# Kernel optimization log

Measured on AMD Instinct MI355X. Metric: run time of the kernel, lower is better.

## Reference

```python
import jax, jax.numpy as jnp
import numpy as np


def setup_inputs() -> dict:
    key = jax.random.key(0)
    k1, k2, k3, k4, k5 = jax.random.split(key, 5)
    B, N, E, C, O = 4, 10000, 32, 128, 128
    x = jax.random.normal(k1, (B, N, C), dtype=jnp.float32)
    idx = jax.random.randint(k2, (B, N, E), 0, N)
    drop = jax.random.uniform(k3, (B, N, E)) < 0.1
    edge_index = jnp.where(drop, -1, idx).astype(jnp.int64)
    W = jax.random.normal(k4, (2 * C, O), dtype=jnp.float32) * (1.0 / np.sqrt(2 * C))
    b = jax.random.normal(k5, (O,), dtype=jnp.float32) * 0.01
    return {"x": x, "edge_index": edge_index, "W": W, "b": b}


def reference(x, edge_index, W, b):
    B, N, C = x.shape
    E = edge_index.shape[-1]
    # pad a zero node row; -1 indices point at it (torch negative-index semantics)
    padded = jnp.concatenate([x, jnp.zeros((B, 1, C), dtype=x.dtype)], axis=1)  # [B, N+1, C]
    idx = jnp.where(edge_index < 0, N, edge_index)
    neigh = jax.vmap(lambda p, i: p[i])(padded, idx)  # [B, N, E, C]
    x_e = jnp.broadcast_to(x[:, :, None, :], (B, N, E, C))
    feat = jnp.concatenate([x_e, neigh - x_e], axis=-1)  # [B, N, E, 2C]
    h = jax.nn.elu(jnp.einsum('bnec,co->bneo', feat, W) + b)  # [B, N, E, O]
    h = jnp.where((edge_index != -1)[..., None], h, -jnp.inf)
    return jnp.max(h, axis=2)  # [B, N, O]
```

## Files before the change

### kernel.cpp

```cpp
#include <hip/hip_runtime.h>
#include <math.h>

#define BATCH 4
#define NNODE 10000
#define EDIM  32
#define CDIM  128
#define ODIM  128
#define MTOT  (BATCH * NNODE)

typedef __attribute__((ext_vector_type(8))) short bf16x8;
typedef __attribute__((ext_vector_type(4))) float f32x4;

__device__ __forceinline__ unsigned short f2bf(float f) {
    unsigned u = __float_as_uint(f);
    u += 0x7fffu + ((u >> 16) & 1u);
    return (unsigned short)(u >> 16);
}
__device__ __forceinline__ float bf2f(unsigned short h) {
    return __uint_as_float(((unsigned)h) << 16);
}

__global__ __launch_bounds__(256) void prep_w(
    const float* __restrict__ W, unsigned short* __restrict__ Bcat,
    unsigned short* __restrict__ Tsent)
{
    int gid = blockIdx.x * 256 + threadIdx.x;
    int n = gid >> 7;
    int k = gid & 127;
    float v;
    if (n < 128) v = W[(size_t)k * ODIM + n] - W[(size_t)(k + 128) * ODIM + n];
    else         v = W[(size_t)(k + 128) * ODIM + (n - 128)];
    Bcat[(size_t)n * CDIM + k] = f2bf(v);
    if (gid < ODIM) Tsent[gid] = 0xFF80;
}

__global__ __launch_bounds__(256) void gemm_mfma(
    const float* __restrict__ x,
    const unsigned short* __restrict__ Bcat,
    const float* __restrict__ bias,
    unsigned short* __restrict__ U,
    unsigned short* __restrict__ T)
{
    __shared__ char lds_raw[32 * 132 * 4];
    unsigned short* As = (unsigned short*)lds_raw;
    float*          Cf = (float*)lds_raw;

    const int tid  = threadIdx.x;
    const int m0   = blockIdx.x * 32;
    const int wv   = tid >> 6;
    const int lane = tid & 63;
    const int l16  = lane & 15;
    const int quad = lane >> 4;
    const int nq   = wv * 64;

    #pragma unroll
    for (int i = 0; i < 4; i++) {
        int lin = i * 256 + tid;
        int row = lin >> 5;
        int f4  = lin & 31;
        float4 v = *(const float4*)&x[(size_t)(m0 + row) * CDIM + f4 * 4];
        ushort4 h;
        h.x = f2bf(v.x); h.y = f2bf(v.y); h.z = f2bf(v.z); h.w = f2bf(v.w);
        int kblk = f4 >> 1, half = f4 & 1;
        *(ushort4*)((char*)As + row * 256 + (((kblk ^ (row & 15)) << 4) + half * 8)) = h;
    }
    __syncthreads();

    f32x4 acc[2][4];
    #pragma unroll
    for (int i = 0; i < 2; i++)
        #pragma unroll
        for (int j = 0; j < 4; j++) acc[i][j] = (f32x4){0.f, 0.f, 0.f, 0.f};

    #pragma unroll
    for (int ks = 0; ks < 4; ks++) {
        const int kb = ks * 32 + quad * 8;

        bf16x8 bfr[4];
        #pragma unroll
        for (int ct = 0; ct < 4; ct++)
            bfr[ct] = *(const bf16x8*)(Bcat + (size_t)(nq + ct * 16 + l16) * CDIM + kb);

        bf16x8 afr[2];
        #pragma unroll
        for (int rt = 0; rt < 2; rt++) {
            int row  = rt * 16 + l16;
            int kblk = ks * 4 + quad;
            afr[rt] = *(const bf16x8*)((char*)As + row * 256 + ((kblk ^ l16) << 4));
        }

        #pragma unroll
        for (int rt = 0; rt < 2; rt++)
            #pragma unroll
            for (int ct = 0; ct < 4; ct++)
                acc[rt][ct] = __builtin_amdgcn_mfma_f32_16x16x32_bf16(
                    afr[rt], bfr[ct], acc[rt][ct], 0, 0, 0);
    }

    __syncthreads();
    if (wv < 2) {
        #pragma unroll
        for (int rt = 0; rt < 2; rt++)
            #pragma unroll
            for (int ct = 0; ct < 4; ct++)
                #pragma unroll
                for (int r = 0; r < 4; r++)
                    Cf[(rt * 16 + quad * 4 + r) * 132 + nq + ct * 16 + l16] = acc[rt][ct][r];
    }
    __syncthreads();
    #pragma unroll
    for (int i = 0; i < 4; i++) {
        int lin = i * 256 + tid;
        int row = lin >> 5, f4 = lin & 31;
        float4 v  = *(const float4*)&Cf[row * 132 + f4 * 4];
        float4 bb = *(const float4*)&bias[f4 * 4];
        ushort4 h;
        h.x = f2bf(v.x + bb.x); h.y = f2bf(v.y + bb.y);
        h.z = f2bf(v.z + bb.z); h.w = f2bf(v.w + bb.w);
        *(ushort4*)&U[(size_t)(m0 + row) * ODIM + f4 * 4] = h;
    }
    __syncthreads();
    if (wv >= 2) {
        #pragma unroll
        for (int rt = 0; rt < 2; rt++)
            #pragma unroll
            for (int ct = 0; ct < 4; ct++)
                #pragma unroll
                for (int r = 0; r < 4; r++)
                    Cf[(rt * 16 + quad * 4 + r) * 132 + (nq - 128) + ct * 16 + l16] = acc[rt][ct][r];
    }
    __syncthreads();
    #pragma unroll
    for (int i = 0; i < 4; i++) {
        int lin = i * 256 + tid;
        int row = lin >> 5, f4 = lin & 31;
        float4 v = *(const float4*)&Cf[row * 132 + f4 * 4];
        ushort4 h;
        h.x = f2bf(v.x); h.y = f2bf(v.y); h.z = f2bf(v.z); h.w = f2bf(v.w);
        *(ushort4*)&T[(size_t)(m0 + row) * ODIM + f4 * 4] = h;
    }
}

__global__ __launch_bounds__(256) void gather_max(
    const int* __restrict__ idx,
    const unsigned short* __restrict__ Ub,
    const unsigned short* __restrict__ T,
    float* __restrict__ out)
{
    __shared__ int sidx[16][EDIM];

    const int g   = blockIdx.x;
    const int b   = g & 3;
    const int nb0 = (g >> 2) * 16;
    const int tid = threadIdx.x;
    const int sent = NNODE * (BATCH - b);

    #pragma unroll
    for (int i = 0; i < 2; i++) {
        int lin = i * 256 + tid;
        int n = lin >> 5, e = lin & 31;
        int j = idx[(size_t)(b * NNODE + nb0 + n) * EDIM + e];
        sidx[n][e] = (j < 0) ? sent : j;
    }
    __syncthreads();

    const int wv   = tid >> 6;
    const int lane = tid & 63;
    const int q4   = lane >> 4;
    const int l16  = lane & 15;
    const int myn  = wv * 4 + q4;
    const int node = b * NNODE + nb0 + myn;
    const unsigned short* tb = T + (size_t)b * NNODE * ODIM;
    const int o8 = l16 * 8;

    uint4 uraw = *(const uint4*)(Ub + (size_t)node * ODIM + o8);

    float m[8];
    #pragma unroll
    for (int i = 0; i < 8; i++) m[i] = -INFINITY;

    #pragma unroll
    for (int e0 = 0; e0 < EDIM; e0 += 16) {
        uint4 v[16];
        #pragma unroll
        for (int q = 0; q < 16; q++) {
            int j = sidx[myn][e0 + q];
            v[q] = *(const uint4*)(tb + (size_t)j * ODIM + o8);
        }
        #pragma unroll
        for (int q = 0; q < 16; q++) {
            m[0] = fmaxf(m[0], __uint_as_float(v[q].x << 16));
            m[1] = fmaxf(m[1], __uint_as_float(v[q].x & 0xffff0000u));
            m[2] = fmaxf(m[2], __uint_as_float(v[q].y << 16));
            m[3] = fmaxf(m[3], __uint_as_float(v[q].y & 0xffff0000u));
            m[4] = fmaxf(m[4], __uint_as_float(v[q].z << 16));
            m[5] = fmaxf(m[5], __uint_as_float(v[q].z & 0xffff0000u));
            m[6] = fmaxf(m[6], __uint_as_float(v[q].w << 16));
            m[7] = fmaxf(m[7], __uint_as_float(v[q].w & 0xffff0000u));
        }
    }

    const bool any = m[0] > -INFINITY;
    float uu[8];
    uu[0] = bf2f((unsigned short)(uraw.x & 0xffff)); uu[1] = bf2f((unsigned short)(uraw.x >> 16));
    uu[2] = bf2f((unsigned short)(uraw.y & 0xffff)); uu[3] = bf2f((unsigned short)(uraw.y >> 16));
    uu[4] = bf2f((unsigned short)(uraw.z & 0xffff)); uu[5] = bf2f((unsigned short)(uraw.z >> 16));
    uu[6] = bf2f((unsigned short)(uraw.w & 0xffff)); uu[7] = bf2f((unsigned short)(uraw.w >> 16));
    float r[8];
    #pragma unroll
    for (int i = 0; i < 8; i++) {
        float s = uu[i] + m[i];
        r[i] = any ? (s > 0.f ? s : __expf(s) - 1.f) : -INFINITY;
    }
    *(float4*)&out[(size_t)node * ODIM + o8]     = make_float4(r[0], r[1], r[2], r[3]);
    *(float4*)&out[(size_t)node * ODIM + o8 + 4] = make_float4(r[4], r[5], r[6], r[7]);
}

extern "C" void kernel_launch(void* const* d_in, const int* in_sizes, int n_in,
                              void* d_out, int out_size, void* d_ws, size_t ws_size,
                              hipStream_t stream) {
    const float* x    = (const float*)d_in[0];
    const int*   idx  = (const int*)d_in[1];
    const float* W    = (const float*)d_in[2];
    const float* bias = (const float*)d_in[3];
    float* out        = (float*)d_out;

    const size_t tBytes = (size_t)(MTOT + 1) * ODIM * sizeof(unsigned short);
    const size_t uBytes = (size_t)MTOT * ODIM * sizeof(unsigned short);
    unsigned short* T    = (unsigned short*)d_ws;
    unsigned short* U    = (unsigned short*)((char*)d_ws + tBytes);
    unsigned short* Bcat = (unsigned short*)((char*)d_ws + tBytes + uBytes);
    unsigned short* Tsent = T + (size_t)MTOT * ODIM;

    prep_w    <<<128,        256, 0, stream>>>(W, Bcat, Tsent);
    gemm_mfma <<<MTOT / 32,  256, 0, stream>>>(x, Bcat, bias, U, T);
    gather_max<<<MTOT / 16,  256, 0, stream>>>(idx, U, T, out);
}
```

Before: 111.3 us.

## Store GEMM results straight from MFMA registers and use packed f16 max in gather

```diff
diff --git a/kernel.cpp b/kernel.cpp
--- a/kernel.cpp
+++ b/kernel.cpp
@@ -11,6 +11,8 @@
 typedef __attribute__((ext_vector_type(8))) short bf16x8;
 typedef __attribute__((ext_vector_type(4))) float f32x4;
 
+#define SENT_BF16 0xFBFFu
+
 __device__ __forceinline__ unsigned short f2bf(float f) {
     unsigned u = __float_as_uint(f);
     u += 0x7fffu + ((u >> 16) & 1u);
@@ -18,6 +20,9 @@
 }
 __device__ __forceinline__ float bf2f(unsigned short h) {
     return __uint_as_float(((unsigned)h) << 16);
+}
+__device__ __forceinline__ void pkmax(unsigned& acc, unsigned v) {
+    asm("v_pk_max_f16 %0, %0, %1" : "+v"(acc) : "v"(v));
 }
 
 __global__ __launch_bounds__(256) void prep_w(
@@ -31,7 +36,7 @@
     if (n < 128) v = W[(size_t)k * ODIM + n] - W[(size_t)(k + 128) * ODIM + n];
     else         v = W[(size_t)(k + 128) * ODIM + (n - 128)];
     Bcat[(size_t)n * CDIM + k] = f2bf(v);
-    if (gid < ODIM) Tsent[gid] = 0xFF80;
+    if (gid < ODIM) Tsent[gid] = (unsigned short)SENT_BF16;
 }
 
 __global__ __launch_bounds__(256) void gemm_mfma(
@@ -41,9 +46,7 @@
     unsigned short* __restrict__ U,
     unsigned short* __restrict__ T)
 {
-    __shared__ char lds_raw[32 * 132 * 4];
-    unsigned short* As = (unsigned short*)lds_raw;
-    float*          Cf = (float*)lds_raw;
+    __shared__ unsigned short As[32 * 128];
 
     const int tid  = threadIdx.x;
     const int m0   = blockIdx.x * 32;
@@ -76,17 +79,17 @@
     for (int ks = 0; ks < 4; ks++) {
         const int kb = ks * 32 + quad * 8;
 
-        bf16x8 bfr[4];
+        bf16x8 wfr[4];
         #pragma unroll
         for (int ct = 0; ct < 4; ct++)
-            bfr[ct] = *(const bf16x8*)(Bcat + (size_t)(nq + ct * 16 + l16) * CDIM + kb);
-
-        bf16x8 afr[2];
+            wfr[ct] = *(const bf16x8*)(Bcat + (size_t)(nq + ct * 16 + l16) * CDIM + kb);
+
+        bf16x8 xfr[2];
         #pragma unroll
         for (int rt = 0; rt < 2; rt++) {
             int row  = rt * 16 + l16;
             int kblk = ks * 4 + quad;
-            afr[rt] = *(const bf16x8*)((char*)As + row * 256 + ((kblk ^ l16) << 4));
+            xfr[rt] = *(const bf16x8*)((char*)As + row * 256 + ((kblk ^ l16) << 4));
         }
 
         #pragma unroll
@@ -94,50 +97,40 @@
             #pragma unroll
             for (int ct = 0; ct < 4; ct++)
                 acc[rt][ct] = __builtin_amdgcn_mfma_f32_16x16x32_bf16(
-                    afr[rt], bfr[ct], acc[rt][ct], 0, 0, 0);
-    }
-
-    __syncthreads();
+                    wfr[ct], xfr[rt], acc[rt][ct], 0, 0, 0);
+    }
+
     if (wv < 2) {
         #pragma unroll
-        for (int rt = 0; rt < 2; rt++)
+        for (int ct = 0; ct < 4; ct++) {
+            int c0 = nq + ct * 16 + quad * 4;
+            float4 b4 = *(const float4*)&bias[c0];
             #pragma unroll
-            for (int ct = 0; ct < 4; ct++)
-                #pragma unroll
-                for (int r = 0; r < 4; r++)
-                    Cf[(rt * 16 + quad * 4 + r) * 132 + nq + ct * 16 + l16] = acc[rt][ct][r];
-    }
-    __syncthreads();
-    #pragma unroll
-    for (int i = 0; i < 4; i++) {
-        int lin = i * 256 + tid;
-        int row = lin >> 5, f4 = lin & 31;
-        float4 v  = *(const float4*)&Cf[row * 132 + f4 * 4];
-        float4 bb = *(const float4*)&bias[f4 * 4];
-        ushort4 h;
-        h.x = f2bf(v.x + bb.x); h.y = f2bf(v.y + bb.y);
-        h.z = f2bf(v.z + bb.z); h.w = f2bf(v.w + bb.w);
-        *(ushort4*)&U[(size_t)(m0 + row) * ODIM + f4 * 4] = h;
-    }
-    __syncthreads();
-    if (wv >= 2) {
-        #pragma unroll
-        for (int rt = 0; rt < 2; rt++)
+            for (int rt = 0; rt < 2; rt++) {
+                int row = m0 + rt * 16 + l16;
+                ushort4 h;
+                h.x = f2bf(acc[rt][ct][0] + b4.x);
+                h.y = f2bf(acc[rt][ct][1] + b4.y);
+                h.z = f2bf(acc[rt][ct][2] + b4.z);
+                h.w = f2bf(acc[rt][ct][3] + b4.w);
+                *(ushort4*)&U[(size_t)row * ODIM + c0] = h;
+            }
+        }
+    } else {
+        #pragma unroll
+        for (int ct = 0; ct < 4; ct++) {
+            int c0 = (nq - 128) + ct * 16 + quad * 4;
             #pragma unroll
-            for (int ct = 0; ct < 4; ct++)
-                #pragma unroll
-                for (int r = 0; r < 4; r++)
-                    Cf[(rt * 16 + quad * 4 + r) * 132 + (nq - 128) + ct * 16 + l16] = acc[rt][ct][r];
-    }
-    __syncthreads();
-    #pragma unroll
-    for (int i = 0; i < 4; i++) {
-        int lin = i * 256 + tid;
-        int row = lin >> 5, f4 = lin & 31;
-        float4 v = *(const float4*)&Cf[row * 132 + f4 * 4];
-        ushort4 h;
-        h.x = f2bf(v.x); h.y = f2bf(v.y); h.z = f2bf(v.z); h.w = f2bf(v.w);
-        *(ushort4*)&T[(size_t)(m0 + row) * ODIM + f4 * 4] = h;
+            for (int rt = 0; rt < 2; rt++) {
+                int row = m0 + rt * 16 + l16;
+                ushort4 h;
+                h.x = f2bf(acc[rt][ct][0]);
+                h.y = f2bf(acc[rt][ct][1]);
+                h.z = f2bf(acc[rt][ct][2]);
+                h.w = f2bf(acc[rt][ct][3]);
+                *(ushort4*)&T[(size_t)row * ODIM + c0] = h;
+            }
+        }
     }
 }
 
@@ -175,9 +168,8 @@
 
     uint4 uraw = *(const uint4*)(Ub + (size_t)node * ODIM + o8);
 
-    float m[8];
-    #pragma unroll
-    for (int i = 0; i < 8; i++) m[i] = -INFINITY;
+    const unsigned SENT2 = (SENT_BF16 << 16) | SENT_BF16;
+    unsigned m01 = SENT2, m23 = SENT2, m45 = SENT2, m67 = SENT2;
 
     #pragma unroll
     for (int e0 = 0; e0 < EDIM; e0 += 16) {
@@ -189,18 +181,19 @@
         }
         #pragma unroll
         for (int q = 0; q < 16; q++) {
-            m[0] = fmaxf(m[0], __uint_as_float(v[q].x << 16));
-            m[1] = fmaxf(m[1], __uint_as_float(v[q].x & 0xffff0000u));
-            m[2] = fmaxf(m[2], __uint_as_float(v[q].y << 16));
-            m[3] = fmaxf(m[3], __uint_as_float(v[q].y & 0xffff0000u));
-            m[4] = fmaxf(m[4], __uint_as_float(v[q].z << 16));
-            m[5] = fmaxf(m[5], __uint_as_float(v[q].z & 0xffff0000u));
-            m[6] = fmaxf(m[6], __uint_as_float(v[q].w << 16));
-            m[7] = fmaxf(m[7], __uint_as_float(v[q].w & 0xffff0000u));
-        }
-    }
-
-    const bool any = m[0] > -INFINITY;
+            pkmax(m01, v[q].x);
+            pkmax(m23, v[q].y);
+            pkmax(m45, v[q].z);
+            pkmax(m67, v[q].w);
+        }
+    }
+
+    const bool any = (m01 & 0xffffu) != SENT_BF16;
+    float m[8];
+    m[0] = bf2f((unsigned short)(m01 & 0xffff)); m[1] = bf2f((unsigned short)(m01 >> 16));
+    m[2] = bf2f((unsigned short)(m23 & 0xffff)); m[3] = bf2f((unsigned short)(m23 >> 16));
+    m[4] = bf2f((unsigned short)(m45 & 0xffff)); m[5] = bf2f((unsigned short)(m45 >> 16));
+    m[6] = bf2f((unsigned short)(m67 & 0xffff)); m[7] = bf2f((unsigned short)(m67 >> 16));
     float uu[8];
     uu[0] = bf2f((unsigned short)(uraw.x & 0xffff)); uu[1] = bf2f((unsigned short)(uraw.x >> 16));
     uu[2] = bf2f((unsigned short)(uraw.y & 0xffff)); uu[3] = bf2f((unsigned short)(uraw.y >> 16));
```

Result: no change. 112.5 us (+1.1%).
